# Kernel optimization log

Measured on AMD Instinct MI355X. Metric: run time of the kernel, lower is better.

Reference implementation:

```python
import jax, jax.numpy as jnp
import numpy as np

N, E, D = 50000, 500000, 128


def layer_norm(x, w, b, eps=1e-5):
    mu = jnp.mean(x, axis=-1, keepdims=True)
    var = jnp.var(x, axis=-1, keepdims=True)
    return (x - mu) * jax.lax.rsqrt(var + eps) * w + b


def setup_inputs() -> dict:
    key = jax.random.key(0)
    ks = jax.random.split(key, 8)
    z = jax.random.normal(ks[0], (N, D), dtype=jnp.float32)
    pot_arcs = jax.random.randint(ks[1], (E, 2), 0, N, dtype=jnp.int64)
    s = 1.0 / np.sqrt(D)
    lin1_w = jax.random.uniform(ks[2], (D, D), jnp.float32, -s, s)
    lin1_b = jax.random.uniform(ks[3], (D,), jnp.float32, -s, s)
    lin2_w = jax.random.uniform(ks[4], (D, D), jnp.float32, -s, s)
    lin2_b = jax.random.uniform(ks[5], (D,), jnp.float32, -s, s)
    bil_w = jax.random.uniform(ks[6], (1, D, D), jnp.float32, -s, s)
    bil_b = jax.random.uniform(ks[7], (1,), jnp.float32, -s, s)
    norm_w = jnp.ones((D,), jnp.float32)
    norm_b = jnp.zeros((D,), jnp.float32)
    return {"z": z, "pot_arcs": pot_arcs, "lin1_w": lin1_w, "lin1_b": lin1_b,
            "lin2_w": lin2_w, "lin2_b": lin2_b, "bil_w": bil_w, "bil_b": bil_b,
            "norm_w": norm_w, "norm_b": norm_b}


def reference(z, pot_arcs, lin1_w, lin1_b, lin2_w, lin2_b, bil_w, bil_b, norm_w, norm_b):
    # shared LayerNorm on all nodes
    zn = layer_norm(z, norm_w, norm_b)                     # [N, D]
    x1 = zn[pot_arcs[:, 0]]                                # [E, D] gather heads
    x2 = zn[pot_arcs[:, 1]]                                # [E, D] gather tails
    # lin -> relu -> layernorm (dropout = identity at eval)
    h1 = layer_norm(jax.nn.relu(x1 @ lin1_w.T + lin1_b), norm_w, norm_b)
    h2 = layer_norm(jax.nn.relu(x2 @ lin2_w.T + lin2_b), norm_w, norm_b)
    # bilinear score: out_e = h1_e^T W h2_e + b, W = bil_w[0]
    score = jnp.einsum('ed,df,ef->e', h1, bil_w[0], h2) + bil_b[0]
    return score                                           # [E]
```

## Files before the change

### kernel.cpp

```cpp
#include <hip/hip_runtime.h>

#define D 128
#define TM 64

typedef __attribute__((ext_vector_type(8))) short short8v;
typedef __attribute__((ext_vector_type(4))) float float4v;

__device__ __forceinline__ unsigned short f2bf(float f) {
    unsigned int u = __float_as_uint(f);
    u += 0x7FFFu + ((u >> 16) & 1u);
    return (unsigned short)(u >> 16);
}
__device__ __forceinline__ float bflo(int u) {
    return __uint_as_float(((unsigned int)u) << 16);
}
__device__ __forceinline__ float bfhi(int u) {
    return __uint_as_float(((unsigned int)u) & 0xFFFF0000u);
}

__global__ __launch_bounds__(256) void wconv(
    const float* __restrict__ w1, const float* __restrict__ w2,
    const float* __restrict__ wb, unsigned short* __restrict__ dst)
{
    int tid = blockIdx.x * 256 + threadIdx.x;
    int w = tid >> 11;
    int r = tid & 2047;
    int l = r & 63;
    int tk = r >> 6;
    int t = tk >> 2, ks = tk & 3;
    int n = t * 16 + (l & 15);
    int k = ks * 32 + (l >> 4) * 8;
    const float* src = (w == 0) ? w1 : (w == 1) ? w2 : wb;
    const float* p = src + n * D + k;
    float4 a = *(const float4*)p;
    float4 b = *(const float4*)(p + 4);
    union { int4 i4; unsigned short u[8]; } pk;
    pk.u[0] = f2bf(a.x); pk.u[1] = f2bf(a.y); pk.u[2] = f2bf(a.z); pk.u[3] = f2bf(a.w);
    pk.u[4] = f2bf(b.x); pk.u[5] = f2bf(b.y); pk.u[6] = f2bf(b.z); pk.u[7] = f2bf(b.w);
    *(int4*)(dst + (size_t)tid * 8) = pk.i4;
}

__global__ __launch_bounds__(256, 4) void node_kernel(
    const float* __restrict__ z,
    const unsigned short* __restrict__ wfrag,
    const float* __restrict__ lin1_b, const float* __restrict__ lin2_b,
    const float* __restrict__ norm_w, const float* __restrict__ norm_b,
    unsigned short* __restrict__ T1, unsigned short* __restrict__ T2,
    int N)
{
    __shared__ unsigned short sa[TM][136];
    __shared__ unsigned short sh[TM][136];

    const int tid   = threadIdx.x;
    const int lane  = tid & 63;
    const int wave  = tid >> 6;
    const int n0    = blockIdx.x * TM;
    const int cg    = lane & 15;
    const int q     = lane >> 4;
    const int rbase = wave * 16;

    {
        const int c = cg * 8;
        float4 nw0 = *(const float4*)(norm_w + c);
        float4 nw1 = *(const float4*)(norm_w + c + 4);
        float4 nb0 = *(const float4*)(norm_b + c);
        float4 nb1 = *(const float4*)(norm_b + c + 4);
        #pragma unroll
        for (int it = 0; it < 4; ++it) {
            int rr = rbase + it * 4 + q;
            int n  = n0 + rr;
            int nc = (n < N) ? n : (N - 1);
            const float* zp = z + (size_t)nc * D + c;
            float4 v0 = *(const float4*)zp;
            float4 v1 = *(const float4*)(zp + 4);
            float s  = v0.x + v0.y + v0.z + v0.w + v1.x + v1.y + v1.z + v1.w;
            float qq = v0.x*v0.x + v0.y*v0.y + v0.z*v0.z + v0.w*v0.w
                     + v1.x*v1.x + v1.y*v1.y + v1.z*v1.z + v1.w*v1.w;
            #pragma unroll
            for (int m = 1; m <= 8; m <<= 1) {
                s  += __shfl_xor(s, m, 64);
                qq += __shfl_xor(qq, m, 64);
            }
            float mu  = s * (1.0f / D);
            float var = qq * (1.0f / D) - mu * mu;
            float rs  = rsqrtf(var + 1e-5f);
            union { int4 i4; unsigned short u[8]; } pk;
            pk.u[0] = f2bf((v0.x - mu) * rs * nw0.x + nb0.x);
            pk.u[1] = f2bf((v0.y - mu) * rs * nw0.y + nb0.y);
            pk.u[2] = f2bf((v0.z - mu) * rs * nw0.z + nb0.z);
            pk.u[3] = f2bf((v0.w - mu) * rs * nw0.w + nb0.w);
            pk.u[4] = f2bf((v1.x - mu) * rs * nw1.x + nb1.x);
            pk.u[5] = f2bf((v1.y - mu) * rs * nw1.y + nb1.y);
            pk.u[6] = f2bf((v1.z - mu) * rs * nw1.z + nb1.z);
            pk.u[7] = f2bf((v1.w - mu) * rs * nw1.w + nb1.w);
            *(int4*)&sa[rr][c] = pk.i4;
        }
    }

    float4v acc1[8], acc2[8];
    #pragma unroll
    for (int t = 0; t < 8; ++t) { acc1[t] = (float4v)(0.0f); acc2[t] = (float4v)(0.0f); }
    #pragma unroll
    for (int ks = 0; ks < 4; ++ks) {
        short8v a = *(const short8v*)&sa[rbase + cg][ks * 32 + q * 8];
        const short8v* wp = (const short8v*)wfrag + ks * 64 + lane;
        #pragma unroll
        for (int t = 0; t < 8; ++t) {
            acc1[t] = __builtin_amdgcn_mfma_f32_16x16x32_bf16(a, wp[t * 256],        acc1[t], 0, 0, 0);
            acc2[t] = __builtin_amdgcn_mfma_f32_16x16x32_bf16(a, wp[t * 256 + 2048], acc2[t], 0, 0, 0);
        }
    }

    float nwv[8], nbv[8];
    #pragma unroll
    for (int t = 0; t < 8; ++t) {
        nwv[t] = norm_w[t * 16 + cg];
        nbv[t] = norm_b[t * 16 + cg];
    }

    auto epilogue = [&](float4v* acc, const float* lb, unsigned short (*dst)[136]) {
        float s[4] = {0, 0, 0, 0}, qs[4] = {0, 0, 0, 0};
        #pragma unroll
        for (int t = 0; t < 8; ++t) {
            float b = lb[t * 16 + cg];
            #pragma unroll
            for (int i = 0; i < 4; ++i) {
                float v = fmaxf(acc[t][i] + b, 0.0f);
                acc[t][i] = v;
                s[i] += v; qs[i] += v * v;
            }
        }
        #pragma unroll
        for (int i = 0; i < 4; ++i) {
            #pragma unroll
            for (int m = 1; m <= 8; m <<= 1) {
                s[i]  += __shfl_xor(s[i], m, 64);
                qs[i] += __shfl_xor(qs[i], m, 64);
            }
            float mu  = s[i] * (1.0f / D);
            float var = qs[i] * (1.0f / D) - mu * mu;
            s[i] = mu; qs[i] = rsqrtf(var + 1e-5f);
        }
        #pragma unroll
        for (int t = 0; t < 8; ++t) {
            #pragma unroll
            for (int i = 0; i < 4; ++i)
                dst[rbase + q * 4 + i][t * 16 + cg] = f2bf((acc[t][i] - s[i]) * qs[i] * nwv[t] + nbv[t]);
        }
    };

    auto copyout = [&](const unsigned short (*S)[136], unsigned short* dst) {
        int r = rbase + (lane >> 2);
        int n = n0 + r;
        if (n < N) {
            #pragma unroll
            for (int j = 0; j < 4; ++j) {
                int c = (lane & 3) * 8 + j * 32;
                *(int4*)(dst + (size_t)n * D + c) = *(const int4*)&S[r][c];
            }
        }
    };

    epilogue(acc1, lin1_b, sh);
    epilogue(acc2, lin2_b, sa);
    copyout(sh, T1);

    #pragma unroll
    for (int t = 0; t < 8; ++t) acc1[t] = (float4v)(0.0f);
    #pragma unroll
    for (int ks = 0; ks < 4; ++ks) {
        short8v a = *(const short8v*)&sa[rbase + cg][ks * 32 + q * 8];
        const short8v* wp = (const short8v*)wfrag + 4096 + ks * 64 + lane;
        #pragma unroll
        for (int t = 0; t < 8; ++t)
            acc1[t] = __builtin_amdgcn_mfma_f32_16x16x32_bf16(a, wp[t * 256], acc1[t], 0, 0, 0);
    }
    #pragma unroll
    for (int t = 0; t < 8; ++t)
        #pragma unroll
        for (int i = 0; i < 4; ++i)
            sh[rbase + q * 4 + i][t * 16 + cg] = f2bf(acc1[t][i]);
    copyout(sh, T2);
}

__global__ __launch_bounds__(256) void arc_kernel(
    const int* __restrict__ arcs,
    const unsigned short* __restrict__ T1,
    const unsigned short* __restrict__ T2,
    const float* __restrict__ bil_b,
    float* __restrict__ out, int E)
{
    const int tid  = threadIdx.x;
    const int lane = tid & 63;
    long long gw = ((long long)blockIdx.x * 256 + tid) >> 6;
    long long e0 = gw * 16;
    int aidx = lane >> 2;
    int s    = lane & 3;

    long long ii = e0 * 2 + (lane & 31);
    long long iimax = (long long)E * 2 - 1;
    int iv = arcs[ii <= iimax ? ii : iimax];
    int a0 = __shfl(iv, aidx * 2, 64);
    int a1 = __shfl(iv, aidx * 2 + 1, 64);
    long long e = e0 + aidx;

    const int4* P = (const int4*)(T1 + (size_t)a0 * D);
    const int4* Q = (const int4*)(T2 + (size_t)a1 * D);
    int4 x0 = P[s];
    int4 x1 = P[s + 4];
    int4 x2 = P[s + 8];
    int4 x3 = P[s + 12];
    int4 y0 = Q[s];
    int4 y1 = Q[s + 4];
    int4 y2 = Q[s + 8];
    int4 y3 = Q[s + 12];

    float acc = 0.0f;
    acc += bflo(x0.x)*bflo(y0.x) + bfhi(x0.x)*bfhi(y0.x);
    acc += bflo(x0.y)*bflo(y0.y) + bfhi(x0.y)*bfhi(y0.y);
    acc += bflo(x0.z)*bflo(y0.z) + bfhi(x0.z)*bfhi(y0.z);
    acc += bflo(x0.w)*bflo(y0.w) + bfhi(x0.w)*bfhi(y0.w);
    acc += bflo(x1.x)*bflo(y1.x) + bfhi(x1.x)*bfhi(y1.x);
    acc += bflo(x1.y)*bflo(y1.y) + bfhi(x1.y)*bfhi(y1.y);
    acc += bflo(x1.z)*bflo(y1.z) + bfhi(x1.z)*bfhi(y1.z);
    acc += bflo(x1.w)*bflo(y1.w) + bfhi(x1.w)*bfhi(y1.w);
    acc += bflo(x2.x)*bflo(y2.x) + bfhi(x2.x)*bfhi(y2.x);
    acc += bflo(x2.y)*bflo(y2.y) + bfhi(x2.y)*bfhi(y2.y);
    acc += bflo(x2.z)*bflo(y2.z) + bfhi(x2.z)*bfhi(y2.z);
    acc += bflo(x2.w)*bflo(y2.w) + bfhi(x2.w)*bfhi(y2.w);
    acc += bflo(x3.x)*bflo(y3.x) + bfhi(x3.x)*bfhi(y3.x);
    acc += bflo(x3.y)*bflo(y3.y) + bfhi(x3.y)*bfhi(y3.y);
    acc += bflo(x3.z)*bflo(y3.z) + bfhi(x3.z)*bfhi(y3.z);
    acc += bflo(x3.w)*bflo(y3.w) + bfhi(x3.w)*bfhi(y3.w);

    acc += __shfl_xor(acc, 1, 64);
    acc += __shfl_xor(acc, 2, 64);

    if (s == 0 && e < E) out[e] = acc + bil_b[0];
}

extern "C" void kernel_launch(void* const* d_in, const int* in_sizes, int n_in,
                              void* d_out, int out_size, void* d_ws, size_t ws_size,
                              hipStream_t stream) {
    const float* z      = (const float*)d_in[0];
    const int*   arcs   = (const int*)d_in[1];
    const float* lin1_w = (const float*)d_in[2];
    const float* lin1_b = (const float*)d_in[3];
    const float* lin2_w = (const float*)d_in[4];
    const float* lin2_b = (const float*)d_in[5];
    const float* bil_w  = (const float*)d_in[6];
    const float* bil_b  = (const float*)d_in[7];
    const float* norm_w = (const float*)d_in[8];
    const float* norm_b = (const float*)d_in[9];
    float* out = (float*)d_out;

    const int N = in_sizes[0] / D;
    const int E = in_sizes[1] / 2;

    unsigned short* wfrag = (unsigned short*)d_ws;
    unsigned short* T1 = wfrag + 3 * 16384;
    unsigned short* T2 = T1 + (size_t)N * D;

    wconv<<<24, 256, 0, stream>>>(lin1_w, lin2_w, bil_w, wfrag);

    node_kernel<<<(N + TM - 1) / TM, 256, 0, stream>>>(
        z, wfrag, lin1_b, lin2_b, norm_w, norm_b, T1, T2, N);

    long long waves = ((long long)E + 15) / 16;
    int blocks = (int)((waves + 3) / 4);
    arc_kernel<<<blocks, 256, 0, stream>>>(arcs, T1, T2, bil_b, out, E);
}
```

Before: 142.4 us.

## Fuse weight conversion, node and arc kernels into one cooperative persistent kernel

Replaces three separate launches with a single cooperative kernel of 1024 blocks that converts the weights, runs the node LayerNorm/GEMM tiles in a grid-stride loop and then the arc scoring, separated by grid-wide syncs. The first layernorm tile is computed before the first sync so it overlaps the weight conversion. This aims to remove kernel launch gaps and tail effects between stages, at the cost of grid.sync overhead and fewer resident blocks per stage. If the cooperative launch fails, it falls back to the original three launches.

```diff
diff --git a/kernel.cpp b/kernel.cpp
--- a/kernel.cpp
+++ b/kernel.cpp
@@ -1,4 +1,7 @@
 #include <hip/hip_runtime.h>
+#include <hip/hip_cooperative_groups.h>
+
+namespace cg = cooperative_groups;
 
 #define D 128
 #define TM 64
@@ -18,11 +21,12 @@
     return __uint_as_float(((unsigned int)u) & 0xFFFF0000u);
 }
 
-__global__ __launch_bounds__(256) void wconv(
-    const float* __restrict__ w1, const float* __restrict__ w2,
+
+__device__ __forceinline__ void wconv_item(
+    int tid, const float* __restrict__ w1, const float* __restrict__ w2,
     const float* __restrict__ wb, unsigned short* __restrict__ dst)
 {
-    int tid = blockIdx.x * 256 + threadIdx.x;
+    if (tid >= 6144) return;
     int w = tid >> 11;
     int r = tid & 2047;
     int l = r & 63;
@@ -40,69 +44,69 @@
     *(int4*)(dst + (size_t)tid * 8) = pk.i4;
 }
 
-__global__ __launch_bounds__(256, 4) void node_kernel(
-    const float* __restrict__ z,
+__device__ __forceinline__ void ln_tile(
+    const float* __restrict__ z, const float* __restrict__ norm_w,
+    const float* __restrict__ norm_b, unsigned short (*sa)[136],
+    int n0, int N, int lane, int wave)
+{
+    const int cg_ = lane & 15;
+    const int q   = lane >> 4;
+    const int rbase = wave * 16;
+    const int c = cg_ * 8;
+    float4 nw0 = *(const float4*)(norm_w + c);
+    float4 nw1 = *(const float4*)(norm_w + c + 4);
+    float4 nb0 = *(const float4*)(norm_b + c);
+    float4 nb1 = *(const float4*)(norm_b + c + 4);
+    #pragma unroll
+    for (int it = 0; it < 4; ++it) {
+        int rr = rbase + it * 4 + q;
+        int n  = n0 + rr;
+        int nc = (n < N) ? n : (N - 1);
+        const float* zp = z + (size_t)nc * D + c;
+        float4 v0 = *(const float4*)zp;
+        float4 v1 = *(const float4*)(zp + 4);
+        float s  = v0.x + v0.y + v0.z + v0.w + v1.x + v1.y + v1.z + v1.w;
+        float qq = v0.x*v0.x + v0.y*v0.y + v0.z*v0.z + v0.w*v0.w
+                 + v1.x*v1.x + v1.y*v1.y + v1.z*v1.z + v1.w*v1.w;
+        #pragma unroll
+        for (int m = 1; m <= 8; m <<= 1) {
+            s  += __shfl_xor(s, m, 64);
+            qq += __shfl_xor(qq, m, 64);
+        }
+        float mu  = s * (1.0f / D);
+        float var = qq * (1.0f / D) - mu * mu;
+        float rs  = rsqrtf(var + 1e-5f);
+        union { int4 i4; unsigned short u[8]; } pk;
+        pk.u[0] = f2bf((v0.x - mu) * rs * nw0.x + nb0.x);
+        pk.u[1] = f2bf((v0.y - mu) * rs * nw0.y + nb0.y);
+        pk.u[2] = f2bf((v0.z - mu) * rs * nw0.z + nb0.z);
+        pk.u[3] = f2bf((v0.w - mu) * rs * nw0.w + nb0.w);
+        pk.u[4] = f2bf((v1.x - mu) * rs * nw1.x + nb1.x);
+        pk.u[5] = f2bf((v1.y - mu) * rs * nw1.y + nb1.y);
+        pk.u[6] = f2bf((v1.z - mu) * rs * nw1.z + nb1.z);
+        pk.u[7] = f2bf((v1.w - mu) * rs * nw1.w + nb1.w);
+        *(int4*)&sa[rr][c] = pk.i4;
+    }
+}
+
+__device__ __forceinline__ void node_rest(
     const unsigned short* __restrict__ wfrag,
     const float* __restrict__ lin1_b, const float* __restrict__ lin2_b,
     const float* __restrict__ norm_w, const float* __restrict__ norm_b,
     unsigned short* __restrict__ T1, unsigned short* __restrict__ T2,
-    int N)
-{
-    __shared__ unsigned short sa[TM][136];
-    __shared__ unsigned short sh[TM][136];
-
-    const int tid   = threadIdx.x;
-    const int lane  = tid & 63;
-    const int wave  = tid >> 6;
-    const int n0    = blockIdx.x * TM;
-    const int cg    = lane & 15;
-    const int q     = lane >> 4;
+    int N, int n0, unsigned short (*sa)[136], unsigned short (*sh)[136],
+    int lane, int wave)
+{
+    const int cg_ = lane & 15;
+    const int q   = lane >> 4;
     const int rbase = wave * 16;
 
-    {
-        const int c = cg * 8;
-        float4 nw0 = *(const float4*)(norm_w + c);
-        float4 nw1 = *(const float4*)(norm_w + c + 4);
-        float4 nb0 = *(const float4*)(norm_b + c);
-        float4 nb1 = *(const float4*)(norm_b + c + 4);
-        #pragma unroll
-        for (int it = 0; it < 4; ++it) {
-            int rr = rbase + it * 4 + q;
-            int n  = n0 + rr;
-            int nc = (n < N) ? n : (N - 1);
-            const float* zp = z + (size_t)nc * D + c;
-            float4 v0 = *(const float4*)zp;
-            float4 v1 = *(const float4*)(zp + 4);
-            float s  = v0.x + v0.y + v0.z + v0.w + v1.x + v1.y + v1.z + v1.w;
-            float qq = v0.x*v0.x + v0.y*v0.y + v0.z*v0.z + v0.w*v0.w
-                     + v1.x*v1.x + v1.y*v1.y + v1.z*v1.z + v1.w*v1.w;
-            #pragma unroll
-            for (int m = 1; m <= 8; m <<= 1) {
-                s  += __shfl_xor(s, m, 64);
-                qq += __shfl_xor(qq, m, 64);
-            }
-            float mu  = s * (1.0f / D);
-            float var = qq * (1.0f / D) - mu * mu;
-            float rs  = rsqrtf(var + 1e-5f);
-            union { int4 i4; unsigned short u[8]; } pk;
-            pk.u[0] = f2bf((v0.x - mu) * rs * nw0.x + nb0.x);
-            pk.u[1] = f2bf((v0.y - mu) * rs * nw0.y + nb0.y);
-            pk.u[2] = f2bf((v0.z - mu) * rs * nw0.z + nb0.z);
-            pk.u[3] = f2bf((v0.w - mu) * rs * nw0.w + nb0.w);
-            pk.u[4] = f2bf((v1.x - mu) * rs * nw1.x + nb1.x);
-            pk.u[5] = f2bf((v1.y - mu) * rs * nw1.y + nb1.y);
-            pk.u[6] = f2bf((v1.z - mu) * rs * nw1.z + nb1.z);
-            pk.u[7] = f2bf((v1.w - mu) * rs * nw1.w + nb1.w);
-            *(int4*)&sa[rr][c] = pk.i4;
-        }
-    }
-
     float4v acc1[8], acc2[8];
     #pragma unroll
     for (int t = 0; t < 8; ++t) { acc1[t] = (float4v)(0.0f); acc2[t] = (float4v)(0.0f); }
     #pragma unroll
     for (int ks = 0; ks < 4; ++ks) {
-        short8v a = *(const short8v*)&sa[rbase + cg][ks * 32 + q * 8];
+        short8v a = *(const short8v*)&sa[rbase + cg_][ks * 32 + q * 8];
         const short8v* wp = (const short8v*)wfrag + ks * 64 + lane;
         #pragma unroll
         for (int t = 0; t < 8; ++t) {
@@ -114,15 +118,15 @@
     float nwv[8], nbv[8];
     #pragma unroll
     for (int t = 0; t < 8; ++t) {
-        nwv[t] = norm_w[t * 16 + cg];
-        nbv[t] = norm_b[t * 16 + cg];
+        nwv[t] = norm_w[t * 16 + cg_];
+        nbv[t] = norm_b[t * 16 + cg_];
     }
 
     auto epilogue = [&](float4v* acc, const float* lb, unsigned short (*dst)[136]) {
         float s[4] = {0, 0, 0, 0}, qs[4] = {0, 0, 0, 0};
         #pragma unroll
         for (int t = 0; t < 8; ++t) {
-            float b = lb[t * 16 + cg];
+            float b = lb[t * 16 + cg_];
             #pragma unroll
             for (int i = 0; i < 4; ++i) {
                 float v = fmaxf(acc[t][i] + b, 0.0f);
@@ -145,7 +149,7 @@
         for (int t = 0; t < 8; ++t) {
             #pragma unroll
             for (int i = 0; i < 4; ++i)
-                dst[rbase + q * 4 + i][t * 16 + cg] = f2bf((acc[t][i] - s[i]) * qs[i] * nwv[t] + nbv[t]);
+                dst[rbase + q * 4 + i][t * 16 + cg_] = f2bf((acc[t][i] - s[i]) * qs[i] * nwv[t] + nbv[t]);
         }
     };
 
@@ -169,7 +173,7 @@
     for (int t = 0; t < 8; ++t) acc1[t] = (float4v)(0.0f);
     #pragma unroll
     for (int ks = 0; ks < 4; ++ks) {
-        short8v a = *(const short8v*)&sa[rbase + cg][ks * 32 + q * 8];
+        short8v a = *(const short8v*)&sa[rbase + cg_][ks * 32 + q * 8];
         const short8v* wp = (const short8v*)wfrag + 4096 + ks * 64 + lane;
         #pragma unroll
         for (int t = 0; t < 8; ++t)
@@ -179,21 +183,17 @@
     for (int t = 0; t < 8; ++t)
         #pragma unroll
         for (int i = 0; i < 4; ++i)
-            sh[rbase + q * 4 + i][t * 16 + cg] = f2bf(acc1[t][i]);
+            sh[rbase + q * 4 + i][t * 16 + cg_] = f2bf(acc1[t][i]);
     copyout(sh, T2);
 }
 
-__global__ __launch_bounds__(256) void arc_kernel(
+__device__ __forceinline__ void arc_tile(
     const int* __restrict__ arcs,
-    const unsigned short* __restrict__ T1,
-    const unsigned short* __restrict__ T2,
-    const float* __restrict__ bil_b,
-    float* __restrict__ out, int E)
-{
-    const int tid  = threadIdx.x;
-    const int lane = tid & 63;
-    long long gw = ((long long)blockIdx.x * 256 + tid) >> 6;
-    long long e0 = gw * 16;
+    const unsigned short* __restrict__ T1, const unsigned short* __restrict__ T2,
+    const float* __restrict__ bil_b, float* __restrict__ out, int E,
+    long long at, int lane, int wave)
+{
+    long long e0 = at * 64 + (long long)wave * 16;
     int aidx = lane >> 2;
     int s    = lane & 3;
 
@@ -239,6 +239,86 @@
     if (s == 0 && e < E) out[e] = acc + bil_b[0];
 }
 
+
+__global__ __launch_bounds__(256, 4) void fused_kernel(
+    const float* __restrict__ z, const int* __restrict__ arcs,
+    const float* __restrict__ w1, const float* __restrict__ w2,
+    const float* __restrict__ wbil,
+    const float* __restrict__ lin1_b, const float* __restrict__ lin2_b,
+    const float* __restrict__ norm_w, const float* __restrict__ norm_b,
+    const float* __restrict__ bil_b,
+    unsigned short* __restrict__ wfrag,
+    unsigned short* __restrict__ T1, unsigned short* __restrict__ T2,
+    float* __restrict__ out, int N, int E)
+{
+    __shared__ unsigned short sa[TM][136];
+    __shared__ unsigned short sh[TM][136];
+
+    const int lane = threadIdx.x & 63;
+    const int wave = threadIdx.x >> 6;
+    const int ntiles = (N + TM - 1) / TM;
+    cg::grid_group grid = cg::this_grid();
+
+    if ((int)blockIdx.x < ntiles)
+        ln_tile(z, norm_w, norm_b, sa, (int)blockIdx.x * TM, N, lane, wave);
+    if (blockIdx.x >= gridDim.x - 24) {
+        int t = (int)(blockIdx.x - (gridDim.x - 24)) * 256 + (int)threadIdx.x;
+        wconv_item(t, w1, w2, wbil, wfrag);
+    }
+    grid.sync();
+
+    if ((int)blockIdx.x < ntiles)
+        node_rest(wfrag, lin1_b, lin2_b, norm_w, norm_b, T1, T2, N,
+                  (int)blockIdx.x * TM, sa, sh, lane, wave);
+    for (int t = (int)blockIdx.x + (int)gridDim.x; t < ntiles; t += (int)gridDim.x) {
+        ln_tile(z, norm_w, norm_b, sa, t * TM, N, lane, wave);
+        node_rest(wfrag, lin1_b, lin2_b, norm_w, norm_b, T1, T2, N,
+                  t * TM, sa, sh, lane, wave);
+    }
+    grid.sync();
+
+    long long natiles = ((long long)E + 63) >> 6;
+    for (long long at = blockIdx.x; at < natiles; at += gridDim.x)
+        arc_tile(arcs, T1, T2, bil_b, out, E, at, lane, wave);
+}
+
+
+__global__ __launch_bounds__(256) void wconv(
+    const float* __restrict__ w1, const float* __restrict__ w2,
+    const float* __restrict__ wb, unsigned short* __restrict__ dst)
+{
+    wconv_item(blockIdx.x * 256 + threadIdx.x, w1, w2, wb, dst);
+}
+
+__global__ __launch_bounds__(256, 4) void node_kernel(
+    const float* __restrict__ z,
+    const unsigned short* __restrict__ wfrag,
+    const float* __restrict__ lin1_b, const float* __restrict__ lin2_b,
+    const float* __restrict__ norm_w, const float* __restrict__ norm_b,
+    unsigned short* __restrict__ T1, unsigned short* __restrict__ T2,
+    int N)
+{
+    __shared__ unsigned short sa[TM][136];
+    __shared__ unsigned short sh[TM][136];
+    const int lane = threadIdx.x & 63;
+    const int wave = threadIdx.x >> 6;
+    ln_tile(z, norm_w, norm_b, sa, blockIdx.x * TM, N, lane, wave);
+    node_rest(wfrag, lin1_b, lin2_b, norm_w, norm_b, T1, T2, N,
+              blockIdx.x * TM, sa, sh, lane, wave);
+}
+
+__global__ __launch_bounds__(256) void arc_kernel(
+    const int* __restrict__ arcs,
+    const unsigned short* __restrict__ T1,
+    const unsigned short* __restrict__ T2,
+    const float* __restrict__ bil_b,
+    float* __restrict__ out, int E)
+{
+    const int lane = threadIdx.x & 63;
+    const int wave = threadIdx.x >> 6;
+    arc_tile(arcs, T1, T2, bil_b, out, E, (long long)blockIdx.x, lane, wave);
+}
+
 extern "C" void kernel_launch(void* const* d_in, const int* in_sizes, int n_in,
                               void* d_out, int out_size, void* d_ws, size_t ws_size,
                               hipStream_t stream) {
@@ -261,12 +341,21 @@
     unsigned short* T1 = wfrag + 3 * 16384;
     unsigned short* T2 = T1 + (size_t)N * D;
 
-    wconv<<<24, 256, 0, stream>>>(lin1_w, lin2_w, bil_w, wfrag);
-
-    node_kernel<<<(N + TM - 1) / TM, 256, 0, stream>>>(
-        z, wfrag, lin1_b, lin2_b, norm_w, norm_b, T1, T2, N);
-
-    long long waves = ((long long)E + 15) / 16;
-    int blocks = (int)((waves + 3) / 4);
-    arc_kernel<<<blocks, 256, 0, stream>>>(arcs, T1, T2, bil_b, out, E);
-}
+    void* kargs[] = {
+        (void*)&z, (void*)&arcs, (void*)&lin1_w, (void*)&lin2_w, (void*)&bil_w,
+        (void*)&lin1_b, (void*)&lin2_b, (void*)&norm_w, (void*)&norm_b, (void*)&bil_b,
+        (void*)&wfrag, (void*)&T1, (void*)&T2, (void*)&out, (void*)&N, (void*)&E
+    };
+    hipError_t err = hipLaunchCooperativeKernel(
+        (const void*)fused_kernel, dim3(1024), dim3(256), kargs, 0, stream);
+
+    if (err != hipSuccess) {
+        (void)hipGetLastError();
+        wconv<<<24, 256, 0, stream>>>(lin1_w, lin2_w, bil_w, wfrag);
+        node_kernel<<<(N + TM - 1) / TM, 256, 0, stream>>>(
+            z, wfrag, lin1_b, lin2_b, norm_w, norm_b, T1, T2, N);
+        long long waves = ((long long)E + 15) / 16;
+        int blocks = (int)((waves + 3) / 4);
+        arc_kernel<<<blocks, 256, 0, stream>>>(arcs, T1, T2, bil_b, out, E);
+    }
+}
```

Result: slower. 412.2 us (+189.5%).
